# Performance work log

Measured on AMD Instinct MI355X. Metric: run time of the kernel, lower is better.

Reference implementation:

```python
import jax, jax.numpy as jnp
import numpy as np

B, C, H, W = 4, 64, 224, 224
WS = 14
HEADS = 4
HD = C // HEADS  # 16
N = WS * WS      # 196
SCALE = HD ** -0.5


def conv2d(x, w, b, pad):
    y = jax.lax.conv_general_dilated(x, w, (1, 1), [(pad, pad), (pad, pad)],
                                     dimension_numbers=('NCHW', 'OIHW', 'NCHW'))
    return y + b[None, :, None, None]


def layernorm(x, g, b, eps=1e-5):
    m = jnp.mean(x, axis=-1, keepdims=True)
    v = jnp.mean((x - m) ** 2, axis=-1, keepdims=True)
    return (x - m) * jax.lax.rsqrt(v + eps) * g + b


def window_partition(x):
    # x: (B,H,W,C) -> (B*nW, WS, WS, C)
    b, h, w, c = x.shape
    x = x.reshape(b, h // WS, WS, w // WS, WS, c)
    return x.transpose(0, 1, 3, 2, 4, 5).reshape(-1, WS, WS, c)


def window_reverse(win, h, w):
    b = win.shape[0] // ((h // WS) * (w // WS))
    x = win.reshape(b, h // WS, w // WS, WS, WS, -1)
    return x.transpose(0, 1, 3, 2, 4, 5).reshape(b, h, w, -1)


def setup_inputs():
    key = jax.random.key(0)
    ks = iter(jax.random.split(key, 64))
    nrm = lambda shp, s=0.02: (jax.random.normal(next(ks), shp, jnp.float32) * s)
    d = {}
    d['x'] = jax.random.normal(next(ks), (B, C, H, W), jnp.float32)
    d['x_basic'] = jax.random.normal(next(ks), (B, C, H, W), jnp.float32)
    # Aware_offset convs
    d['c1_w'] = nrm((64, 64, 3, 3)); d['c1_b'] = jnp.zeros((64,), jnp.float32)
    d['c2_w'] = nrm((64, 64, 5, 5)); d['c2_b'] = jnp.zeros((64,), jnp.float32)
    d['c3_w'] = nrm((64, 64, 7, 7)); d['c3_b'] = jnp.zeros((64,), jnp.float32)
    d['c4_w'] = nrm((64, 192, 3, 3)); d['c4_b'] = jnp.zeros((64,), jnp.float32)
    d['c5_w'] = nrm((128, 128, 3, 3)); d['c5_b'] = jnp.zeros((128,), jnp.float32)
    d['c6_w'] = nrm((128, 128, 3, 3)); d['c6_b'] = jnp.zeros((128,), jnp.float32)
    d['c7_w'] = nrm((64, 128, 1, 1)); d['c7_b'] = jnp.zeros((64,), jnp.float32)
    d['c8_w'] = nrm((64, 128, 1, 1)); d['c8_b'] = jnp.zeros((64,), jnp.float32)
    # block params
    d['qkv1_w'] = nrm((64, 64, 3, 3)); d['qkv1_b'] = jnp.zeros((64,), jnp.float32)
    d['n1_g'] = jnp.ones((C,), jnp.float32); d['n1_b'] = jnp.zeros((C,), jnp.float32)
    d['qkv_w'] = nrm((3 * C, C)); d['qkv_b'] = jnp.zeros((3 * C,), jnp.float32)
    d['corr_w'] = nrm((N, HD)); d['corr_b'] = jnp.zeros((N,), jnp.float32)
    d['proj_w'] = nrm((C, C)); d['proj_b'] = jnp.zeros((C,), jnp.float32)
    d['n2_g'] = jnp.ones((C,), jnp.float32); d['n2_b'] = jnp.zeros((C,), jnp.float32)
    d['fc1_w'] = nrm((2 * C, C)); d['fc1_b'] = jnp.zeros((2 * C,), jnp.float32)
    d['fc2_w'] = nrm((C, 2 * C)); d['fc2_b'] = jnp.zeros((C,), jnp.float32)
    return d


def _forward(x, x_basic, c1_w, c1_b, c2_w, c2_b, c3_w, c3_b, c4_w, c4_b,
             c5_w, c5_b, c6_w, c6_b, c7_w, c7_b, c8_w, c8_b,
             qkv1_w, qkv1_b, n1_g, n1_b, qkv_w, qkv_b, corr_w, corr_b,
             proj_w, proj_b, n2_g, n2_b, fc1_w, fc1_b, fc2_w, fc2_b):
    relu = jax.nn.relu
    # ---- Aware_offset ----
    in1 = relu(conv2d(x, c1_w, c1_b, 1))
    in2 = relu(conv2d(x, c2_w, c2_b, 2))
    in3 = relu(conv2d(x, c3_w, c3_b, 3))
    xo = relu(conv2d(jnp.concatenate([in1, in2, in3], 1), c4_w, c4_b, 1))
    cat12 = jnp.concatenate([x, x_basic], 1)
    b1 = relu(conv2d(cat12, c5_w, c5_b, 1))
    b2 = jax.nn.sigmoid(relu(conv2d(b1, c6_w, c6_b, 1)))
    b1 = relu(conv2d(b1 * b2, c7_w, c7_b, 0))
    xb = xo * b1 + relu(conv2d(cat12, c8_w, c8_b, 0))  # (B,C,H,W)
    xb = xb.transpose(0, 2, 3, 1)                       # (B,H,W,C)
    # ---- pre-attn: norm1 + convQKV1 ----
    xt = x.reshape(B, C, H * W).transpose(0, 2, 1)      # (B,L,C)
    xt = layernorm(xt, n1_g, n1_b)
    xc = xt.reshape(B, H, W, C).transpose(0, 3, 1, 2)
    xc = conv2d(xc, qkv1_w, qkv1_b, 1).transpose(0, 2, 3, 1)  # (B,H,W,C)
    # ---- windows ----
    xw = window_partition(xc).reshape(-1, N, C)   # (B_,N,C)
    xbw = window_partition(xb).reshape(-1, N, C)
    B_ = xw.shape[0]
    # ---- window attention with correction bias ----
    qkv = (xw @ qkv_w.T + qkv_b).reshape(B_, N, 3, HEADS, HD).transpose(2, 0, 3, 1, 4)
    q, k, v = qkv[0] * SCALE, qkv[1], qkv[2]            # (B_,h,N,hd)
    xcorr = xbw.reshape(B_, N, HEADS, HD).transpose(0, 2, 1, 3)
    xcorr = xcorr @ corr_w.T + corr_b                   # (B_,h,N,196)
    attn = jax.nn.softmax(jnp.einsum('bhnd,bhmd->bhnm', q, k) + xcorr, axis=-1)
    out = jnp.einsum('bhnm,bhmd->bhnd', attn, v).transpose(0, 2, 1, 3).reshape(B_, N, C)
    out = out @ proj_w.T + proj_b
    # ---- reverse + MLP ----
    sx = window_reverse(out.reshape(-1, WS, WS, C), H, W)  # (B,H,W,C)
    xt = sx.reshape(B, H * W, C)
    h = layernorm(xt, n2_g, n2_b)
    h = jax.nn.gelu(h @ fc1_w.T + fc1_b, approximate=False) @ fc2_w.T + fc2_b
    xt = xt + h
    return xt.reshape(B, H, W, C).transpose(0, 3, 1, 2)


def reference(x, x_basic, c1_w, c1_b, c2_w, c2_b, c3_w, c3_b, c4_w, c4_b,
              c5_w, c5_b, c6_w, c6_b, c7_w, c7_b, c8_w, c8_b,
              qkv1_w, qkv1_b, n1_g, n1_b, qkv_w, qkv_b, corr_w, corr_b,
              proj_w, proj_b, n2_g, n2_b, fc1_w, fc1_b, fc2_w, fc2_b):
    return _forward(x, x_basic, c1_w, c1_b, c2_w, c2_b, c3_w, c3_b, c4_w, c4_b,
                    c5_w, c5_b, c6_w, c6_b, c7_w, c7_b, c8_w, c8_b,
                    qkv1_w, qkv1_b, n1_g, n1_b, qkv_w, qkv_b, corr_w, corr_b,
                    proj_w, proj_b, n2_g, n2_b, fc1_w, fc1_b, fc2_w, fc2_b)
```

## Files before the change

### kernel.cpp

```cpp
#include <hip/hip_runtime.h>
#include <hip/hip_bf16.h>
#include <math.h>


#define HW  50176
#define WID 224

typedef unsigned short ushortT;
typedef __attribute__((ext_vector_type(8))) short bf8_t;
typedef __attribute__((ext_vector_type(4))) short bf4_t;
typedef __attribute__((ext_vector_type(4))) float f4_t;

__device__ __forceinline__ ushortT f2bf(float v) {
    __hip_bfloat16 h = __float2bfloat16(v);
    ushortT u; __builtin_memcpy(&u, &h, 2); return u;
}
__device__ __forceinline__ float bf2f(ushortT h) {
    union { float f; unsigned int u; } c; c.u = ((unsigned int)h) << 16;
    return c.f;
}
__device__ __forceinline__ void cvt8(const float* xv, bf8_t& hh, bf8_t& ll) {
    #pragma unroll
    for (int i = 0; i < 8; ++i) {
        ushortT hi = f2bf(xv[i]);
        hh[i] = (short)hi;
        ll[i] = (short)f2bf(xv[i] - bf2f(hi));
    }
}

__global__ __launch_bounds__(256) void packw(
    const float* __restrict__ w, ushortT* __restrict__ dst,
    int K, int IC, int OC, int total)
{
    int e = blockIdx.x * 256 + threadIdx.x;
    if (e >= total) return;
    int KK = K * K;
    int kk = e % KK; int rem = e / KK;
    int ic = rem % IC; int oc = rem / IC;
    float v = w[e];
    ushortT hi = f2bf(v);
    ushortT lo = f2bf(v - bf2f(hi));
    int g = oc >> 6, oc64 = oc & 63;
    int ic32 = ic >> 5, icin = ic & 31, kb = icin >> 3, ii = icin & 7;
    int nch = KK * (IC / 32);
    int chunk = ic32 * KK + kk;
    size_t base = ((size_t)(g * nch + chunk)) * 4096;
    dst[base + (kb * 64 + oc64) * 8 + ii] = hi;
    dst[base + 2048 + (kb * 64 + oc64) * 8 + ii] = lo;
}

template<int K>
__device__ __forceinline__ void convpass(
    const ushortT* __restrict__ wq, const ushortT* __restrict__ sm,
    int wv, int lc, int kb, f4_t (&ac)[2][4])
{
    constexpr int off = 3 - K / 2;
    constexpr int INSH = 14 * 22 * 40;
    const int boff = (kb * 64 + lc) * 8;
    bf8_t bh[4], bl[4];
    #pragma unroll
    for (int n = 0; n < 4; ++n) {
        bh[n] = *(const bf8_t*)(wq + boff + n * 128);
        bl[n] = *(const bf8_t*)(wq + 2048 + boff + n * 128);
    }
    #pragma unroll 1
    for (int kk = 0; kk < K * K; ++kk) {
        bf8_t cbh[4], cbl[4];
        #pragma unroll
        for (int n = 0; n < 4; ++n) { cbh[n] = bh[n]; cbl[n] = bl[n]; }
        if (kk + 1 < K * K) {
            const ushortT* wn = wq + (size_t)(kk + 1) * 4096;
            #pragma unroll
            for (int n = 0; n < 4; ++n) {
                bh[n] = *(const bf8_t*)(wn + boff + n * 128);
                bl[n] = *(const bf8_t*)(wn + 2048 + boff + n * 128);
            }
        }
        const int ky = kk / K, kx = kk % K;
        #pragma unroll
        for (int m = 0; m < 2; ++m) {
            const int row = 2 * wv + m + ky + off;
            const int col = lc + kx + off;
            const ushortT* ab = sm + (row * 22 + col) * 40 + kb * 8;
            bf8_t Ah = *(const bf8_t*)ab;
            bf8_t Al = *(const bf8_t*)(ab + INSH);
            #pragma unroll
            for (int n = 0; n < 4; ++n) {
                ac[m][n] = __builtin_amdgcn_mfma_f32_16x16x32_bf16(Ah, cbh[n], ac[m][n], 0, 0, 0);
                ac[m][n] = __builtin_amdgcn_mfma_f32_16x16x32_bf16(Ah, cbl[n], ac[m][n], 0, 0, 0);
                ac[m][n] = __builtin_amdgcn_mfma_f32_16x16x32_bf16(Al, cbh[n], ac[m][n], 0, 0, 0);
            }
        }
    }
}

__global__ __launch_bounds__(256, 4) void mfconv3(
    const float* __restrict__ in,
    const ushortT* __restrict__ w1p, const ushortT* __restrict__ w2p,
    const ushortT* __restrict__ w3p,
    const float* __restrict__ b1, const float* __restrict__ b2,
    const float* __restrict__ b3,
    float* __restrict__ out, int inStride, int outStride)
{
    constexpr int TWd = 22, THd = 14, ICP = 40;
    constexpr int INSH = THd * TWd * ICP;
    constexpr int E = THd * TWd * 32;
    __shared__ __align__(16) ushortT smem_u[2 * INSH];
    float* pool = (float*)smem_u;

    const int t = threadIdx.x, lane = t & 63, wv = t >> 6;
    const int lc = lane & 15, kb = lane >> 4;
    const int img = blockIdx.z;
    const int x0 = blockIdx.x * 16, y0 = blockIdx.y * 8;
    const float* inb = in + (size_t)img * inStride;

    f4_t acc1[2][4], acc2[2][4], acc3[2][4];
    {
        #pragma unroll
        for (int n = 0; n < 4; ++n) {
            float z1 = b1[n * 16 + lc], z2 = b2[n * 16 + lc], z3 = b3[n * 16 + lc];
            #pragma unroll
            for (int m = 0; m < 2; ++m) {
                acc1[m][n] = (f4_t){z1, z1, z1, z1};
                acc2[m][n] = (f4_t){z2, z2, z2, z2};
                acc3[m][n] = (f4_t){z3, z3, z3, z3};
            }
        }
    }

    #pragma unroll 1
    for (int ic32 = 0; ic32 < 2; ++ic32) {
        __syncthreads();
        #pragma unroll 1
        for (int ib = 0; ib < E; ib += 1024) {
            float v[4];
            #pragma unroll
            for (int u = 0; u < 4; ++u) {
                int i = ib + u * 256 + t;
                v[u] = 0.f;
                if (i < E) {
                    int icn = i / (THd * TWd);
                    int px  = i % (THd * TWd);
                    int ty = px / TWd, tx = px % TWd;
                    int gy = y0 + ty - 3, gx = x0 + tx - 3;
                    if (gy >= 0 && gy < WID && gx >= 0 && gx < WID)
                        v[u] = inb[(size_t)(ic32 * 32 + icn) * HW + gy * WID + gx];
                }
            }
            #pragma unroll
            for (int u = 0; u < 4; ++u) {
                int i = ib + u * 256 + t;
                if (i < E) {
                    int icn = i / (THd * TWd);
                    int px  = i % (THd * TWd);
                    ushortT hi = f2bf(v[u]);
                    smem_u[px * ICP + icn] = hi;
                    smem_u[INSH + px * ICP + icn] = f2bf(v[u] - bf2f(hi));
                }
            }
        }
        __syncthreads();
        convpass<3>(w1p + (size_t)(ic32 *  9) * 4096, smem_u, wv, lc, kb, acc1);
        convpass<5>(w2p + (size_t)(ic32 * 25) * 4096, smem_u, wv, lc, kb, acc2);
        convpass<7>(w3p + (size_t)(ic32 * 49) * 4096, smem_u, wv, lc, kb, acc3);
    }

    #pragma unroll 1
    for (int c = 0; c < 3; ++c) {
        float* ob0 = out + (size_t)img * outStride + (size_t)(c * 64) * HW;
        #pragma unroll
        for (int m = 0; m < 2; ++m) {
            __syncthreads();
            #pragma unroll
            for (int n = 0; n < 4; ++n)
                #pragma unroll
                for (int j = 0; j < 4; ++j) {
                    float v = (c == 0) ? acc1[m][n][j] : (c == 1) ? acc2[m][n][j] : acc3[m][n][j];
                    v = fmaxf(v, 0.f);
                    pool[(wv * 64 + n * 16 + lc) * 20 + kb * 4 + j] = v;
                }
            __syncthreads();
            {
                int rho = t >> 6, oc = t & 63;
                int y = y0 + 2 * rho + m;
                float* ob = ob0 + (size_t)oc * HW + (size_t)y * WID + x0;
                const float* pr = &pool[(rho * 64 + oc) * 20];
                #pragma unroll
                for (int c4 = 0; c4 < 4; ++c4) {
                    float4 st = { pr[c4*4+0], pr[c4*4+1], pr[c4*4+2], pr[c4*4+3] };
                    *(float4*)&ob[c4 * 4] = st;
                }
            }
        }
    }
}

template<int K, int IC, int OC, int ACT, bool CAT, bool LNRM, bool NHWCOUT>
__global__ __launch_bounds__(256, 4) void mfconv(
    const float* __restrict__ in, const float* __restrict__ in2,
    const ushortT* __restrict__ wpk, const float* __restrict__ bias,
    const float* __restrict__ mu, const float* __restrict__ rs,
    const float* __restrict__ lng, const float* __restrict__ lnb,
    float* __restrict__ out, int inStride, int outStride)
{
    constexpr int P = K / 2, TWd = 16 + K - 1, THd = 8 + K - 1, ICP = 40;
    constexpr int OCG = OC / 64, KK = K * K, NCH = KK * (IC / 32);
    constexpr int INSH = THd * TWd * ICP;
    constexpr int E = THd * TWd * 32;
    constexpr int SMU = (2 * INSH > 10240) ? 2 * INSH : 10240;
    __shared__ __align__(16) ushortT smem_u[SMU];
    float* pool = (float*)smem_u;

    const int t = threadIdx.x, lane = t & 63, wv = t >> 6;
    const int lc = lane & 15, kb = lane >> 4;
    const int img = blockIdx.z / OCG, g = blockIdx.z % OCG;
    const int x0 = blockIdx.x * 16, y0 = blockIdx.y * 8;
    const float* inb  = in + (size_t)img * inStride;
    const float* in2b = CAT ? (in2 + (size_t)img * inStride) : nullptr;
    const int imgPixBase = img * HW;
    const ushortT* wq0 = wpk + (size_t)g * NCH * 4096;

    f4_t acc[2][4];
    {
        float bz0 = bias[g * 64 +  0 + lc];
        float bz1 = bias[g * 64 + 16 + lc];
        float bz2 = bias[g * 64 + 32 + lc];
        float bz3 = bias[g * 64 + 48 + lc];
        #pragma unroll
        for (int m = 0; m < 2; ++m) {
            acc[m][0] = (f4_t){bz0, bz0, bz0, bz0};
            acc[m][1] = (f4_t){bz1, bz1, bz1, bz1};
            acc[m][2] = (f4_t){bz2, bz2, bz2, bz2};
            acc[m][3] = (f4_t){bz3, bz3, bz3, bz3};
        }
    }
    const int aoff = lc * ICP + kb * 8;
    const int boff = (kb * 64 + lc) * 8;

    #pragma unroll 1
    for (int ic32 = 0; ic32 < IC / 32; ++ic32) {
        __syncthreads();
        #pragma unroll 1
        for (int ib = 0; ib < E; ib += 1024) {
            float v[4];
            #pragma unroll
            for (int u = 0; u < 4; ++u) {
                int i = ib + u * 256 + t;
                v[u] = 0.f;
                if (i < E) {
                    int icn = i / (THd * TWd);
                    int px  = i % (THd * TWd);
                    int ty = px / TWd, tx = px % TWd;
                    int gy = y0 + ty - P, gx = x0 + tx - P;
                    int ic = ic32 * 32 + icn;
                    if (gy >= 0 && gy < WID && gx >= 0 && gx < WID) {
                        const float* s;
                        if (CAT) s = (ic < 64) ? (inb + (size_t)ic * HW)
                                               : (in2b + (size_t)(ic - 64) * HW);
                        else     s = inb + (size_t)ic * HW;
                        float vv = s[gy * WID + gx];
                        if (LNRM) {
                            int p = imgPixBase + gy * WID + gx;
                            vv = (vv - mu[p]) * rs[p] * lng[ic] + lnb[ic];
                        }
                        v[u] = vv;
                    }
                }
            }
            #pragma unroll
            for (int u = 0; u < 4; ++u) {
                int i = ib + u * 256 + t;
                if (i < E) {
                    int icn = i / (THd * TWd);
                    int px  = i % (THd * TWd);
                    ushortT hi = f2bf(v[u]);
                    smem_u[px * ICP + icn] = hi;
                    smem_u[INSH + px * ICP + icn] = f2bf(v[u] - bf2f(hi));
                }
            }
        }
        __syncthreads();
        const ushortT* wqb = wq0 + (size_t)(ic32 * KK) * 4096;
        bf8_t bh[4], bl[4];
        #pragma unroll
        for (int n = 0; n < 4; ++n) {
            bh[n] = *(const bf8_t*)(wqb + boff + n * 128);
            bl[n] = *(const bf8_t*)(wqb + 2048 + boff + n * 128);
        }
        #pragma unroll 1
        for (int kk = 0; kk < KK; ++kk) {
            bf8_t cbh[4], cbl[4];
            #pragma unroll
            for (int n = 0; n < 4; ++n) { cbh[n] = bh[n]; cbl[n] = bl[n]; }
            if (kk + 1 < KK) {
                const ushortT* wn = wqb + (size_t)(kk + 1) * 4096;
                #pragma unroll
                for (int n = 0; n < 4; ++n) {
                    bh[n] = *(const bf8_t*)(wn + boff + n * 128);
                    bl[n] = *(const bf8_t*)(wn + 2048 + boff + n * 128);
                }
            }
            const int ky = kk / K, kx = kk % K;
            #pragma unroll
            for (int m = 0; m < 2; ++m) {
                const int row = 2 * wv + m + ky;
                const ushortT* ab = smem_u + (row * TWd + kx) * ICP + aoff;
                bf8_t Ah = *(const bf8_t*)ab;
                bf8_t Al = *(const bf8_t*)(ab + INSH);
                #pragma unroll
                for (int n = 0; n < 4; ++n) {
                    acc[m][n] = __builtin_amdgcn_mfma_f32_16x16x32_bf16(Ah, cbh[n], acc[m][n], 0, 0, 0);
                    acc[m][n] = __builtin_amdgcn_mfma_f32_16x16x32_bf16(Ah, cbl[n], acc[m][n], 0, 0, 0);
                    acc[m][n] = __builtin_amdgcn_mfma_f32_16x16x32_bf16(Al, cbh[n], acc[m][n], 0, 0, 0);
                }
            }
        }
    }
    if (NHWCOUT) {
        float* ob0 = out + (size_t)img * outStride;
        #pragma unroll
        for (int m = 0; m < 2; ++m) {
            __syncthreads();
            #pragma unroll
            for (int n = 0; n < 4; ++n)
                #pragma unroll
                for (int j = 0; j < 4; ++j) {
                    float v = acc[m][n][j];
                    if (ACT == 1) v = fmaxf(v, 0.f);
                    else if (ACT == 2) v = 1.f / (1.f + __expf(-fmaxf(v, 0.f)));
                    pool[(wv * 16 + kb * 4 + j) * 68 + n * 16 + lc] = v;
                }
            __syncthreads();
            {
                int pix = t >> 2, q = t & 3;
                int y = y0 + 2 * (pix >> 4) + m;
                int x = x0 + (pix & 15);
                float* pr = ob0 + ((size_t)y * WID + x) * 64 + q * 16;
                const float* src = &pool[pix * 68 + q * 16];
                #pragma unroll
                for (int u = 0; u < 4; ++u)
                    *(float4*)&pr[u * 4] = *(const float4*)&src[u * 4];
            }
        }
    } else {
        float* ob0 = out + (size_t)img * outStride + (size_t)(g * 64) * HW;
        #pragma unroll
        for (int m = 0; m < 2; ++m) {
            __syncthreads();
            #pragma unroll
            for (int n = 0; n < 4; ++n)
                #pragma unroll
                for (int j = 0; j < 4; ++j) {
                    float v = acc[m][n][j];
                    if (ACT == 1) v = fmaxf(v, 0.f);
                    else if (ACT == 2) v = 1.f / (1.f + __expf(-fmaxf(v, 0.f)));
                    pool[(wv * 64 + n * 16 + lc) * 20 + kb * 4 + j] = v;
                }
            __syncthreads();
            {
                int rho = t >> 6, oc = t & 63;
                int y = y0 + 2 * rho + m;
                float* ob = ob0 + (size_t)oc * HW + (size_t)y * WID + x0;
                const float* pr = &pool[(rho * 64 + oc) * 20];
                #pragma unroll
                for (int c4 = 0; c4 < 4; ++c4) {
                    float4 st = { pr[c4*4+0], pr[c4*4+1], pr[c4*4+2], pr[c4*4+3] };
                    *(float4*)&ob[c4 * 4] = st;
                }
            }
        }
    }
}

__global__ __launch_bounds__(256) void ln_stats(
    const float* __restrict__ x, float* __restrict__ mu, float* __restrict__ rs)
{
    const int p = blockIdx.x * 256 + threadIdx.x;
    const int img = p / HW, pp = p - img * HW;
    const float* b = x + (size_t)img * 64 * HW + pp;
    float row[64];
    #pragma unroll
    for (int c = 0; c < 64; ++c) row[c] = b[(size_t)c * HW];
    float s1 = 0.f;
    #pragma unroll
    for (int c = 0; c < 64; ++c) s1 += row[c];
    float m = s1 * (1.f / 64.f);
    float s2 = 0.f;
    #pragma unroll
    for (int c = 0; c < 64; ++c) { float d = row[c] - m; s2 += d * d; }
    mu[p] = m;
    rs[p] = rsqrtf(s2 * (1.f / 64.f) + 1e-5f);
}

__global__ __launch_bounds__(256) void xb1x1(
    const float* __restrict__ x, const float* __restrict__ xbas,
    const float* __restrict__ xo, const float* __restrict__ b1, const float* __restrict__ b2,
    const float* __restrict__ c7w, const float* __restrict__ c7b,
    const float* __restrict__ c8w, const float* __restrict__ c8b,
    float* __restrict__ xbout)
{
    __shared__ __align__(16) float w7s[128 * 36], w8s[128 * 36];
    const int t = threadIdx.x, oh = blockIdx.y;
    for (int i = t; i < 4096; i += 256) {
        int o = i >> 7, ic = i & 127;
        w7s[ic * 36 + o] = c7w[(size_t)(oh * 32 + o) * 128 + ic];
        w8s[ic * 36 + o] = c8w[(size_t)(oh * 32 + o) * 128 + ic];
    }
    __syncthreads();
    const int p = blockIdx.x * 256 + t;
    const int img = p / HW, pp = p - img * HW;
    const float* b1p = b1 + (size_t)img * 128 * HW + pp;
    const float* b2p = b2 + (size_t)img * 128 * HW + pp;
    const float* xp  = x  + (size_t)img * 64 * HW + pp;
    const float* xbp = xbas + (size_t)img * 64 * HW + pp;
    float a7[32], a8[32];
    {
        const float4* c74 = (const float4*)(c7b + oh * 32);
        const float4* c84 = (const float4*)(c8b + oh * 32);
        #pragma unroll
        for (int j4 = 0; j4 < 8; ++j4) {
            float4 v7 = c74[j4], v8 = c84[j4];
            a7[j4*4+0]=v7.x; a7[j4*4+1]=v7.y; a7[j4*4+2]=v7.z; a7[j4*4+3]=v7.w;
            a8[j4*4+0]=v8.x; a8[j4*4+1]=v8.y; a8[j4*4+2]=v8.z; a8[j4*4+3]=v8.w;
        }
    }
    #pragma unroll 4
    for (int ic = 0; ic < 128; ++ic) {
        float tv = b1p[(size_t)ic * HW] * b2p[(size_t)ic * HW];
        float cv = (ic < 64) ? xp[(size_t)ic * HW] : xbp[(size_t)(ic - 64) * HW];
        const float4* w7r = (const float4*)&w7s[ic * 36];
        const float4* w8r = (const float4*)&w8s[ic * 36];
        #pragma unroll
        for (int j4 = 0; j4 < 8; ++j4) {
            float4 v7 = w7r[j4], v8 = w8r[j4];
            a7[j4*4+0] = fmaf(tv, v7.x, a7[j4*4+0]);
            a7[j4*4+1] = fmaf(tv, v7.y, a7[j4*4+1]);
            a7[j4*4+2] = fmaf(tv, v7.z, a7[j4*4+2]);
            a7[j4*4+3] = fmaf(tv, v7.w, a7[j4*4+3]);
            a8[j4*4+0] = fmaf(cv, v8.x, a8[j4*4+0]);
            a8[j4*4+1] = fmaf(cv, v8.y, a8[j4*4+1]);
            a8[j4*4+2] = fmaf(cv, v8.z, a8[j4*4+2]);
            a8[j4*4+3] = fmaf(cv, v8.w, a8[j4*4+3]);
        }
    }
    const float* xop = xo + (size_t)img * 64 * HW + pp;
    float* orow = xbout + (size_t)p * 64 + oh * 32;
    #pragma unroll
    for (int j4 = 0; j4 < 8; ++j4) {
        float4 st;
        st.x = xop[(size_t)(oh*32 + j4*4+0) * HW] * fmaxf(a7[j4*4+0], 0.f) + fmaxf(a8[j4*4+0], 0.f);
        st.y = xop[(size_t)(oh*32 + j4*4+1) * HW] * fmaxf(a7[j4*4+1], 0.f) + fmaxf(a8[j4*4+1], 0.f);
        st.z = xop[(size_t)(oh*32 + j4*4+2) * HW] * fmaxf(a7[j4*4+2], 0.f) + fmaxf(a8[j4*4+2], 0.f);
        st.w = xop[(size_t)(oh*32 + j4*4+3) * HW] * fmaxf(a7[j4*4+3], 0.f) + fmaxf(a8[j4*4+3], 0.f);
        *(float4*)&orow[j4 * 4] = st;
    }
}

__global__ __launch_bounds__(256) void attn(
    const float* __restrict__ xc, const float* __restrict__ xb,
    const float* __restrict__ qkvw, const float* __restrict__ qkvb,
    const float* __restrict__ corw, const float* __restrict__ corb,
    float* __restrict__ aout)
{
    constexpr int QS = 40;
    constexpr int VS = 212;
    __shared__ __align__(16) ushortT Kth[196 * QS];
    __shared__ __align__(16) ushortT Ktl[196 * QS];
    __shared__ __align__(16) ushortT Vth[16 * VS];
    __shared__ __align__(16) ushortT Vtl[16 * VS];
    __shared__ __align__(16) float CB[208];

    const int t = threadIdx.x;
    const int wdw = blockIdx.x >> 2, h = blockIdx.x & 3;
    const int b = wdw >> 8, wl = wdw & 255;
    const int wy = (wl >> 4) * 14, wx = (wl & 15) * 14;
    const int lane = t & 63, wv = t >> 6;
    const int g = lane >> 4, col = lane & 15;

    bf8_t Wqh[2], Wql[2], Wkh[2], Wkl[2], Wvh[2], Wvl[2];
    float qb[4], kb[4], vb[4];
    {
        #pragma unroll
        for (int ks = 0; ks < 2; ++ks) {
            float xv[8];
            const float* wr = qkvw + (h * 16 + col) * 64 + ks * 32 + g * 8;
            *(float4*)&xv[0] = *(const float4*)wr;
            *(float4*)&xv[4] = *(const float4*)(wr + 4);
            cvt8(xv, Wqh[ks], Wql[ks]);
            wr = qkvw + (64 + h * 16 + col) * 64 + ks * 32 + g * 8;
            *(float4*)&xv[0] = *(const float4*)wr;
            *(float4*)&xv[4] = *(const float4*)(wr + 4);
            cvt8(xv, Wkh[ks], Wkl[ks]);
            wr = qkvw + (128 + h * 16 + col) * 64 + ks * 32 + g * 8;
            *(float4*)&xv[0] = *(const float4*)wr;
            *(float4*)&xv[4] = *(const float4*)(wr + 4);
            cvt8(xv, Wvh[ks], Wvl[ks]);
        }
        float4 q4 = *(const float4*)(qkvb + h * 16 + g * 4);
        float4 k4 = *(const float4*)(qkvb + 64 + h * 16 + g * 4);
        float4 v4 = *(const float4*)(qkvb + 128 + h * 16 + g * 4);
        qb[0]=q4.x; qb[1]=q4.y; qb[2]=q4.z; qb[3]=q4.w;
        kb[0]=k4.x; kb[1]=k4.y; kb[2]=k4.z; kb[3]=k4.w;
        vb[0]=v4.x; vb[1]=v4.y; vb[2]=v4.z; vb[3]=v4.w;
    }

    if (t < 208) CB[t] = (t < 196) ? corb[t] : 0.f;
    if (t < 196) {
        unsigned* khr = (unsigned*)&Kth[t * QS];
        unsigned* klr = (unsigned*)&Ktl[t * QS];
        float xw[16];
        const float4* cw4 = (const float4*)(corw + t * 16);
        #pragma unroll
        for (int j = 0; j < 4; ++j) *(float4*)&xw[j * 4] = cw4[j];
        #pragma unroll
        for (int i = 0; i < 8; ++i) {
            ushortT ah = f2bf(xw[2*i]), bh = f2bf(xw[2*i+1]);
            ushortT al = f2bf(xw[2*i] - bf2f(ah)), bl = f2bf(xw[2*i+1] - bf2f(bh));
            khr[8 + i] = (unsigned)ah | ((unsigned)bh << 16);
            klr[8 + i] = (unsigned)al | ((unsigned)bl << 16);
        }
    }

    auto phaseB = [&](int mt) -> f4_t {
        const int row = 16 * mt + col;
        const int pix = (row > 195) ? 195 : row;
        const int rr = pix / 14, cc = pix - (pix / 14) * 14;
        const float* xr = xc + (size_t)((b * 224 + wy + rr) * 224 + wx + cc) * 64;
        f4_t dq = (f4_t){0.f, 0.f, 0.f, 0.f};
        f4_t dk = (f4_t){0.f, 0.f, 0.f, 0.f};
        f4_t dv = (f4_t){0.f, 0.f, 0.f, 0.f};
        #pragma unroll
        for (int ks = 0; ks < 2; ++ks) {
            float xv[8];
            *(float4*)&xv[0] = *(const float4*)(xr + ks * 32 + g * 8);
            *(float4*)&xv[4] = *(const float4*)(xr + ks * 32 + g * 8 + 4);
            bf8_t Xh, Xl;
            cvt8(xv, Xh, Xl);
            dq = __builtin_amdgcn_mfma_f32_16x16x32_bf16(Wqh[ks], Xh, dq, 0, 0, 0);
            dq = __builtin_amdgcn_mfma_f32_16x16x32_bf16(Wqh[ks], Xl, dq, 0, 0, 0);
            dq = __builtin_amdgcn_mfma_f32_16x16x32_bf16(Wql[ks], Xh, dq, 0, 0, 0);
            dk = __builtin_amdgcn_mfma_f32_16x16x32_bf16(Wkh[ks], Xh, dk, 0, 0, 0);
            dk = __builtin_amdgcn_mfma_f32_16x16x32_bf16(Wkh[ks], Xl, dk, 0, 0, 0);
            dk = __builtin_amdgcn_mfma_f32_16x16x32_bf16(Wkl[ks], Xh, dk, 0, 0, 0);
            dv = __builtin_amdgcn_mfma_f32_16x16x32_bf16(Wvh[ks], Xh, dv, 0, 0, 0);
            dv = __builtin_amdgcn_mfma_f32_16x16x32_bf16(Wvh[ks], Xl, dv, 0, 0, 0);
            dv = __builtin_amdgcn_mfma_f32_16x16x32_bf16(Wvl[ks], Xh, dv, 0, 0, 0);
        }
        #pragma unroll
        for (int j = 0; j < 4; ++j) {
            float v = dv[j] + vb[j];
            ushortT hi = f2bf(v);
            Vth[(g * 4 + j) * VS + row] = hi;
            Vtl[(g * 4 + j) * VS + row] = f2bf(v - bf2f(hi));
        }
        if (row < 196) {
            unsigned h0, h1, l0, l1;
            {
                float a = dk[0] + kb[0], bb = dk[1] + kb[1];
                ushortT ah = f2bf(a), bh = f2bf(bb);
                h0 = (unsigned)ah | ((unsigned)bh << 16);
                l0 = (unsigned)f2bf(a - bf2f(ah)) | ((unsigned)f2bf(bb - bf2f(bh)) << 16);
            }
            {
                float a = dk[2] + kb[2], bb = dk[3] + kb[3];
                ushortT ah = f2bf(a), bh = f2bf(bb);
                h1 = (unsigned)ah | ((unsigned)bh << 16);
                l1 = (unsigned)f2bf(a - bf2f(ah)) | ((unsigned)f2bf(bb - bf2f(bh)) << 16);
            }
            uint2 u;
            u.x = h0; u.y = h1; *(uint2*)&Kth[row * QS + g * 4] = u;
            u.x = l0; u.y = l1; *(uint2*)&Ktl[row * QS + g * 4] = u;
        }
        return (f4_t){(dq[0] + qb[0]) * 0.25f, (dq[1] + qb[1]) * 0.25f,
                      (dq[2] + qb[2]) * 0.25f, (dq[3] + qb[3]) * 0.25f};
    };

    f4_t dqs0 = phaseB(wv);
    f4_t dqs1 = phaseB(wv + 4);
    f4_t dqs2 = phaseB(wv + 8);
    f4_t dqs3 = (f4_t){0.f, 0.f, 0.f, 0.f};
    if (wv == 0) dqs3 = phaseB(12);
    __syncthreads();

    auto phaseC = [&](f4_t dqv, int qt) {
        const int row = 16 * qt + col;
        const int pixq = (row > 195) ? 195 : row;
        float q8[8];
        const int sl0 = ((2 * g) & 3) * 16 + col;
        const int sl1 = ((2 * g + 1) & 3) * 16 + col;
        q8[0] = __shfl(dqv[0], sl0); q8[1] = __shfl(dqv[1], sl0);
        q8[2] = __shfl(dqv[2], sl0); q8[3] = __shfl(dqv[3], sl0);
        q8[4] = __shfl(dqv[0], sl1); q8[5] = __shfl(dqv[1], sl1);
        q8[6] = __shfl(dqv[2], sl1); q8[7] = __shfl(dqv[3], sl1);
        if (g >= 2) {
            const int rr = pixq / 14, cc = pixq - (pixq / 14) * 14;
            const float* xr = xb + (size_t)((b * 224 + wy + rr) * 224 + wx + cc) * 64
                            + h * 16 + (g & 1) * 8;
            *(float4*)&q8[0] = *(const float4*)xr;
            *(float4*)&q8[4] = *(const float4*)(xr + 4);
        }
        bf8_t Bhf, Blf;
        cvt8(q8, Bhf, Blf);
        f4_t s[13];
        __builtin_amdgcn_s_setprio(1);
        #pragma unroll
        for (int kt = 0; kt < 13; ++kt) {
            const int krow = (16 * kt + col > 195) ? 195 : (16 * kt + col);
            const bf8_t Ahf = *(const bf8_t*)&Kth[krow * QS + g * 8];
            const bf8_t Alf = *(const bf8_t*)&Ktl[krow * QS + g * 8];
            f4_t a = (f4_t){0.f, 0.f, 0.f, 0.f};
            a = __builtin_amdgcn_mfma_f32_16x16x32_bf16(Ahf, Bhf, a, 0, 0, 0);
            a = __builtin_amdgcn_mfma_f32_16x16x32_bf16(Ahf, Blf, a, 0, 0, 0);
            a = __builtin_amdgcn_mfma_f32_16x16x32_bf16(Alf, Bhf, a, 0, 0, 0);
            const f4_t cb4 = *(const f4_t*)&CB[16 * kt + g * 4];
            s[kt] = a + cb4;
        }
        __builtin_amdgcn_s_setprio(0);
        if (g > 0) { s[12][0] = -3e38f; s[12][1] = -3e38f; s[12][2] = -3e38f; s[12][3] = -3e38f; }
        float mrow = -3e38f;
        #pragma unroll
        for (int kt = 0; kt < 13; ++kt)
            #pragma unroll
            for (int j = 0; j < 4; ++j) mrow = fmaxf(mrow, s[kt][j]);
        mrow = fmaxf(mrow, __shfl_xor(mrow, 16));
        mrow = fmaxf(mrow, __shfl_xor(mrow, 32));
        float lsum = 0.f;
        bf4_t ph[13], pl[13];
        #pragma unroll
        for (int kt = 0; kt < 13; ++kt) {
            #pragma unroll
            for (int j = 0; j < 4; ++j) {
                float p = __expf(s[kt][j] - mrow);
                lsum += p;
                ushortT hi = f2bf(p);
                ph[kt][j] = (short)hi;
                pl[kt][j] = (short)f2bf(p - bf2f(hi));
            }
        }
        lsum += __shfl_xor(lsum, 16);
        lsum += __shfl_xor(lsum, 32);
        f4_t o = (f4_t){0.f, 0.f, 0.f, 0.f};
        __builtin_amdgcn_s_setprio(1);
        #pragma unroll
        for (int kt = 0; kt < 13; ++kt) {
            const bf4_t vh = *(const bf4_t*)&Vth[col * VS + 16 * kt + g * 4];
            const bf4_t vl = *(const bf4_t*)&Vtl[col * VS + 16 * kt + g * 4];
            o = __builtin_amdgcn_mfma_f32_16x16x16bf16_1k(vh, ph[kt], o, 0, 0, 0);
            o = __builtin_amdgcn_mfma_f32_16x16x16bf16_1k(vl, ph[kt], o, 0, 0, 0);
            o = __builtin_amdgcn_mfma_f32_16x16x16bf16_1k(vh, pl[kt], o, 0, 0, 0);
        }
        __builtin_amdgcn_s_setprio(0);
        const int pix = 16 * qt + col;
        if (pix < 196) {
            const float inv = 1.f / lsum;
            const int rr = pix / 14, cc = pix % 14;
            const size_t pixIdx = (size_t)((b * 224 + wy + rr) * 224 + wx + cc);
            float4 st = { o[0] * inv, o[1] * inv, o[2] * inv, o[3] * inv };
            *(float4*)&aout[pixIdx * 64 + h * 16 + g * 4] = st;
        }
    };

    phaseC(dqs0, wv);
    phaseC(dqs1, wv + 4);
    phaseC(dqs2, wv + 8);
    if (wv == 0) phaseC(dqs3, 12);
}

__global__ __launch_bounds__(256) void mlpproj(
    const float* __restrict__ aout,
    const float* __restrict__ pw, const float* __restrict__ pbias,
    const float* __restrict__ g, const float* __restrict__ be,
    const float* __restrict__ fc1w, const float* __restrict__ fc1b,
    const float* __restrict__ fc2w, const float* __restrict__ fc2b,
    float* __restrict__ out)
{
    __shared__ __align__(16) float pwT[64 * 68];
    __shared__ __align__(16) float w1[4096], w2t[4096];
    const int t = threadIdx.x;
    for (int i = t; i < 4096; i += 256) {
        int o = i >> 6, c = i & 63;
        pwT[c * 68 + o] = pw[i];
    }
    __syncthreads();
    const int p = blockIdx.x * 256 + t;
    const float* ar = aout + (size_t)p * 64;
    float srow[64];
    {
        const float4* pb4 = (const float4*)pbias;
        #pragma unroll
        for (int j4 = 0; j4 < 16; ++j4) {
            float4 v = pb4[j4];
            srow[j4*4+0]=v.x; srow[j4*4+1]=v.y; srow[j4*4+2]=v.z; srow[j4*4+3]=v.w;
        }
    }
    const float4* ar4 = (const float4*)ar;
    #pragma unroll 2
    for (int c4 = 0; c4 < 16; ++c4) {
        float4 av = ar4[c4];
        const float4* w0 = (const float4*)&pwT[(c4 * 4 + 0) * 68];
        const float4* wB = (const float4*)&pwT[(c4 * 4 + 1) * 68];
        const float4* wC = (const float4*)&pwT[(c4 * 4 + 2) * 68];
        const float4* wD = (const float4*)&pwT[(c4 * 4 + 3) * 68];
        #pragma unroll
        for (int j4 = 0; j4 < 16; ++j4) {
            float4 a0 = w0[j4], a1 = wB[j4], a2 = wC[j4], a3 = wD[j4];
            srow[j4*4+0] = fmaf(av.x, a0.x, fmaf(av.y, a1.x, fmaf(av.z, a2.x, fmaf(av.w, a3.x, srow[j4*4+0]))));
            srow[j4*4+1] = fmaf(av.x, a0.y, fmaf(av.y, a1.y, fmaf(av.z, a2.y, fmaf(av.w, a3.y, srow[j4*4+1]))));
            srow[j4*4+2] = fmaf(av.x, a0.z, fmaf(av.y, a1.z, fmaf(av.z, a2.z, fmaf(av.w, a3.z, srow[j4*4+2]))));
            srow[j4*4+3] = fmaf(av.x, a0.w, fmaf(av.y, a1.w, fmaf(av.z, a2.w, fmaf(av.w, a3.w, srow[j4*4+3]))));
        }
    }
    float s1 = 0.f;
    #pragma unroll
    for (int c = 0; c < 64; ++c) s1 += srow[c];
    float m = s1 * (1.f / 64.f);
    float s2 = 0.f;
    #pragma unroll
    for (int c = 0; c < 64; ++c) { float d = srow[c] - m; s2 += d * d; }
    float rstd = rsqrtf(s2 * (1.f / 64.f) + 1e-5f);
    float nrow[64];
    {
        const float4* g4 = (const float4*)g;
        const float4* b4 = (const float4*)be;
        #pragma unroll
        for (int j4 = 0; j4 < 16; ++j4) {
            float4 gv = g4[j4], bv = b4[j4];
            nrow[j4*4+0] = (srow[j4*4+0] - m) * rstd * gv.x + bv.x;
            nrow[j4*4+1] = (srow[j4*4+1] - m) * rstd * gv.y + bv.y;
            nrow[j4*4+2] = (srow[j4*4+2] - m) * rstd * gv.z + bv.z;
            nrow[j4*4+3] = (srow[j4*4+3] - m) * rstd * gv.w + bv.w;
        }
    }
    float acc[64];
    {
        const float4* f2b4 = (const float4*)fc2b;
        #pragma unroll
        for (int j4 = 0; j4 < 16; ++j4) {
            float4 v = f2b4[j4];
            acc[j4*4+0]=v.x; acc[j4*4+1]=v.y; acc[j4*4+2]=v.z; acc[j4*4+3]=v.w;
        }
    }
    for (int half = 0; half < 2; ++half) {
        __syncthreads();
        for (int i = t; i < 4096; i += 256) {
            int j = i >> 6, c = i & 63;
            w1[i]  = fc1w[(half * 64 + j) * 64 + c];
            w2t[i] = fc2w[c * 128 + half * 64 + j];
        }
        __syncthreads();
        #pragma unroll 1
        for (int j = 0; j < 64; ++j) {
            const float4* wr = (const float4*)&w1[j * 64];
            float d0 = 0, d1 = 0, d2 = 0, d3 = 0;
            #pragma unroll
            for (int c4 = 0; c4 < 16; ++c4) {
                float4 wv = wr[c4];
                d0 = fmaf(nrow[c4*4+0], wv.x, d0); d1 = fmaf(nrow[c4*4+1], wv.y, d1);
                d2 = fmaf(nrow[c4*4+2], wv.z, d2); d3 = fmaf(nrow[c4*4+3], wv.w, d3);
            }
            float hv = fc1b[half * 64 + j] + ((d0 + d1) + (d2 + d3));
            float gl = 0.5f * hv * (1.f + erff(hv * 0.70710678118f));
            const float4* w2r = (const float4*)&w2t[j * 64];
            #pragma unroll
            for (int c4 = 0; c4 < 16; ++c4) {
                float4 wv = w2r[c4];
                acc[c4*4+0] = fmaf(gl, wv.x, acc[c4*4+0]);
                acc[c4*4+1] = fmaf(gl, wv.y, acc[c4*4+1]);
                acc[c4*4+2] = fmaf(gl, wv.z, acc[c4*4+2]);
                acc[c4*4+3] = fmaf(gl, wv.w, acc[c4*4+3]);
            }
        }
    }
    const int img = p / HW, pp = p - img * HW;
    float* ob = out + (size_t)img * 64 * HW + pp;
    #pragma unroll
    for (int c = 0; c < 64; ++c)
        ob[(size_t)c * HW] = srow[c] + acc[c];
}

extern "C" void kernel_launch(void* const* d_in, const int* in_sizes, int n_in,
                              void* d_out, int out_size, void* d_ws, size_t ws_size,
                              hipStream_t stream)
{
    (void)in_sizes; (void)n_in; (void)out_size;
    const float* x      = (const float*)d_in[0];
    const float* xbasic = (const float*)d_in[1];
    const float* c1w  = (const float*)d_in[2];  const float* c1b  = (const float*)d_in[3];
    const float* c2w  = (const float*)d_in[4];  const float* c2b  = (const float*)d_in[5];
    const float* c3w  = (const float*)d_in[6];  const float* c3b  = (const float*)d_in[7];
    const float* c4w  = (const float*)d_in[8];  const float* c4b  = (const float*)d_in[9];
    const float* c5w  = (const float*)d_in[10]; const float* c5b  = (const float*)d_in[11];
    const float* c6w  = (const float*)d_in[12]; const float* c6b  = (const float*)d_in[13];
    const float* c7w  = (const float*)d_in[14]; const float* c7b  = (const float*)d_in[15];
    const float* c8w  = (const float*)d_in[16]; const float* c8b  = (const float*)d_in[17];
    const float* qk1w = (const float*)d_in[18]; const float* qk1b = (const float*)d_in[19];
    const float* n1g  = (const float*)d_in[20]; const float* n1b  = (const float*)d_in[21];
    const float* qkvw = (const float*)d_in[22]; const float* qkvb = (const float*)d_in[23];
    const float* corw = (const float*)d_in[24]; const float* corb = (const float*)d_in[25];
    const float* prjw = (const float*)d_in[26]; const float* prjb = (const float*)d_in[27];
    const float* n2g  = (const float*)d_in[28]; const float* n2b  = (const float*)d_in[29];
    const float* f1w  = (const float*)d_in[30]; const float* f1b  = (const float*)d_in[31];
    const float* f2w  = (const float*)d_in[32]; const float* f2b  = (const float*)d_in[33];

    float* ws = (float*)d_ws;
    const size_t SCR0 = 26836992ull;
    const size_t need4 = (SCR0 + 4ull * 19267584ull) * 4ull;
    const size_t need2 = (SCR0 + 2ull * 19267584ull) * 4ull;
    const int CS = (ws_size >= need4) ? 4 : (ws_size >= need2) ? 2 : 1;
    const int nch = 4 / CS;

    float* XC = ws;
    float* XB = ws + 12845056;
    float* MU = ws + 25690112;
    float* RS = ws + 25890816;
    ushortT* WP = (ushortT*)(ws + 26091520);
    float* A  = ws + SCR0;
    float* XO = A + (size_t)CS * 9633792;
    float* B1 = XO + (size_t)CS * 3211264;
    float* B2 = A;
    float* AOUT = A;
    ushortT* WQ1 = (ushortT*)B1;

    const size_t o1 = 0, o2 = 73728, o3 = 278528, o4 = 679936, o5 = 901120, o6 = 1196032;

    ln_stats<<<784, 256, 0, stream>>>(x, MU, RS);

    {
        auto PK = [&](const float* w, ushortT* dst, int K, int IC, int OC) {
            int tot = OC * IC * K * K;
            packw<<<(tot + 255) / 256, 256, 0, stream>>>(w, dst, K, IC, OC, tot);
        };
        PK(qk1w, WQ1, 3, 64, 64);
        PK(c1w, WP + o1, 3, 64, 64);
        PK(c2w, WP + o2, 5, 64, 64);
        PK(c3w, WP + o3, 7, 64, 64);
        PK(c4w, WP + o4, 3, 192, 64);
        PK(c5w, WP + o5, 3, 128, 128);
        PK(c6w, WP + o6, 3, 128, 128);
    }

    mfconv<3, 64, 64, 0, false, true, true><<<dim3(14, 28, 4), 256, 0, stream>>>(
        x, nullptr, WQ1, qk1b, MU, RS, n1g, n1b, XC, 64 * HW, HW * 64);

    for (int ch = 0; ch < nch; ++ch) {
        const float* xi  = x      + (size_t)ch * CS * 64 * HW;
        const float* xbi = xbasic + (size_t)ch * CS * 64 * HW;
        mfconv3<<<dim3(14, 28, CS), 256, 0, stream>>>(
            xi, WP + o1, WP + o2, WP + o3, c1b, c2b, c3b, A, 64 * HW, 192 * HW);
        mfconv<3, 192, 64, 1, false, false, false><<<dim3(14, 28, CS), 256, 0, stream>>>(
            A, nullptr, WP + o4, c4b, nullptr, nullptr, nullptr, nullptr, XO, 192 * HW, 64 * HW);
        mfconv<3, 128, 128, 1, true, false, false><<<dim3(14, 28, CS * 2), 256, 0, stream>>>(
            xi, xbi, WP + o5, c5b, nullptr, nullptr, nullptr, nullptr, B1, 64 * HW, 128 * HW);
        mfconv<3, 128, 128, 2, false, false, false><<<dim3(14, 28, CS * 2), 256, 0, stream>>>(
            B1, nullptr, WP + o6, c6b, nullptr, nullptr, nullptr, nullptr, B2, 128 * HW, 128 * HW);
        xb1x1<<<dim3(CS * 196, 2), 256, 0, stream>>>(
            xi, xbi, XO, B1, B2, c7w, c7b, c8w, c8b, XB + (size_t)ch * CS * HW * 64);
    }

    attn<<<4096, 256, 0, stream>>>(XC, XB, qkvw, qkvb, corw, corb, AOUT);
    mlpproj<<<784, 256, 0, stream>>>(AOUT, prjw, prjb, n2g, n2b, f1w, f1b, f2w, f2b,
                                     (float*)d_out);
}
```

Measured before the change: 1.917 ms.

## Rewrite proj+LN+MLP tail on MFMA with split-bf16 prepacked weights

Replaces the scalar-FMA per-pixel projection, LayerNorm and GELU MLP kernel with an MFMA version. Each wave handles 16 pixels and uses split-bf16 (hi/lo, three products) to keep near-fp32 accuracy. The LayerNorm reduction moves to cross-lane shuffles, and the weights are prepacked into MFMA fragment layout by new small pack kernels, stored in the freed MU buffer. The aim is to cut the large VALU cost of the three 64/128-wide matmuls. In exchange it adds extra MFMA work for the split precision, plus strided output stores.

After: 1.778 ms (median of 2 runs). 1.08x faster.

```diff
diff --git a/kernel.cpp b/kernel.cpp
--- a/kernel.cpp
+++ b/kernel.cpp
@@ -47,6 +47,36 @@
     size_t base = ((size_t)(g * nch + chunk)) * 4096;
     dst[base + (kb * 64 + oc64) * 8 + ii] = hi;
     dst[base + 2048 + (kb * 64 + oc64) * 8 + ii] = lo;
+}
+
+__global__ __launch_bounds__(256) void packa32(
+    const float* __restrict__ w, ushortT* __restrict__ dst, int K, int total)
+{
+    int e = blockIdx.x * 256 + threadIdx.x;
+    if (e >= total) return;
+    int f = e >> 9, r = e & 511, ln = r >> 3, i = r & 7;
+    int nk = K >> 5;
+    int o = f / nk, ks = f % nk;
+    int c = ln & 15, gg = ln >> 4;
+    float v = w[(size_t)(o * 16 + c) * K + ks * 32 + gg * 8 + i];
+    ushortT hi = f2bf(v);
+    dst[(size_t)f * 1024 + ln * 8 + i] = hi;
+    dst[(size_t)f * 1024 + 512 + ln * 8 + i] = f2bf(v - bf2f(hi));
+}
+
+__global__ __launch_bounds__(256) void packa16(
+    const float* __restrict__ w, ushortT* __restrict__ dst, int K, int total)
+{
+    int e = blockIdx.x * 256 + threadIdx.x;
+    if (e >= total) return;
+    int f = e >> 8, r = e & 255, ln = r >> 2, i = r & 3;
+    int nk = K >> 4;
+    int o = f / nk, n = f % nk;
+    int c = ln & 15, gg = ln >> 4;
+    float v = w[(size_t)(o * 16 + c) * K + n * 16 + gg * 4 + i];
+    ushortT hi = f2bf(v);
+    dst[(size_t)f * 512 + ln * 4 + i] = hi;
+    dst[(size_t)f * 512 + 256 + ln * 4 + i] = f2bf(v - bf2f(hi));
 }
 
 template<int K>
@@ -666,116 +696,120 @@
     if (wv == 0) phaseC(dqs3, 12);
 }
 
-__global__ __launch_bounds__(256) void mlpproj(
-    const float* __restrict__ aout,
-    const float* __restrict__ pw, const float* __restrict__ pbias,
-    const float* __restrict__ g, const float* __restrict__ be,
-    const float* __restrict__ fc1w, const float* __restrict__ fc1b,
-    const float* __restrict__ fc2w, const float* __restrict__ fc2b,
+__global__ __launch_bounds__(256) void mlpmf(
+    const float* __restrict__ aout, const ushortT* __restrict__ pk,
+    const float* __restrict__ pbias,
+    const float* __restrict__ lng, const float* __restrict__ lnb,
+    const float* __restrict__ fc1b, const float* __restrict__ fc2b,
     float* __restrict__ out)
 {
-    __shared__ __align__(16) float pwT[64 * 68];
-    __shared__ __align__(16) float w1[4096], w2t[4096];
-    const int t = threadIdx.x;
-    for (int i = t; i < 4096; i += 256) {
-        int o = i >> 6, c = i & 63;
-        pwT[c * 68 + o] = pw[i];
-    }
-    __syncthreads();
-    const int p = blockIdx.x * 256 + t;
-    const float* ar = aout + (size_t)p * 64;
-    float srow[64];
-    {
-        const float4* pb4 = (const float4*)pbias;
-        #pragma unroll
-        for (int j4 = 0; j4 < 16; ++j4) {
-            float4 v = pb4[j4];
-            srow[j4*4+0]=v.x; srow[j4*4+1]=v.y; srow[j4*4+2]=v.z; srow[j4*4+3]=v.w;
-        }
-    }
-    const float4* ar4 = (const float4*)ar;
-    #pragma unroll 2
-    for (int c4 = 0; c4 < 16; ++c4) {
-        float4 av = ar4[c4];
-        const float4* w0 = (const float4*)&pwT[(c4 * 4 + 0) * 68];
-        const float4* wB = (const float4*)&pwT[(c4 * 4 + 1) * 68];
-        const float4* wC = (const float4*)&pwT[(c4 * 4 + 2) * 68];
-        const float4* wD = (const float4*)&pwT[(c4 * 4 + 3) * 68];
-        #pragma unroll
-        for (int j4 = 0; j4 < 16; ++j4) {
-            float4 a0 = w0[j4], a1 = wB[j4], a2 = wC[j4], a3 = wD[j4];
-            srow[j4*4+0] = fmaf(av.x, a0.x, fmaf(av.y, a1.x, fmaf(av.z, a2.x, fmaf(av.w, a3.x, srow[j4*4+0]))));
-            srow[j4*4+1] = fmaf(av.x, a0.y, fmaf(av.y, a1.y, fmaf(av.z, a2.y, fmaf(av.w, a3.y, srow[j4*4+1]))));
-            srow[j4*4+2] = fmaf(av.x, a0.z, fmaf(av.y, a1.z, fmaf(av.z, a2.z, fmaf(av.w, a3.z, srow[j4*4+2]))));
-            srow[j4*4+3] = fmaf(av.x, a0.w, fmaf(av.y, a1.w, fmaf(av.z, a2.w, fmaf(av.w, a3.w, srow[j4*4+3]))));
-        }
-    }
-    float s1 = 0.f;
-    #pragma unroll
-    for (int c = 0; c < 64; ++c) s1 += srow[c];
-    float m = s1 * (1.f / 64.f);
-    float s2 = 0.f;
-    #pragma unroll
-    for (int c = 0; c < 64; ++c) { float d = srow[c] - m; s2 += d * d; }
-    float rstd = rsqrtf(s2 * (1.f / 64.f) + 1e-5f);
-    float nrow[64];
-    {
-        const float4* g4 = (const float4*)g;
-        const float4* b4 = (const float4*)be;
-        #pragma unroll
-        for (int j4 = 0; j4 < 16; ++j4) {
-            float4 gv = g4[j4], bv = b4[j4];
-            nrow[j4*4+0] = (srow[j4*4+0] - m) * rstd * gv.x + bv.x;
-            nrow[j4*4+1] = (srow[j4*4+1] - m) * rstd * gv.y + bv.y;
-            nrow[j4*4+2] = (srow[j4*4+2] - m) * rstd * gv.z + bv.z;
-            nrow[j4*4+3] = (srow[j4*4+3] - m) * rstd * gv.w + bv.w;
-        }
-    }
-    float acc[64];
-    {
-        const float4* f2b4 = (const float4*)fc2b;
-        #pragma unroll
-        for (int j4 = 0; j4 < 16; ++j4) {
-            float4 v = f2b4[j4];
-            acc[j4*4+0]=v.x; acc[j4*4+1]=v.y; acc[j4*4+2]=v.z; acc[j4*4+3]=v.w;
-        }
-    }
-    for (int half = 0; half < 2; ++half) {
-        __syncthreads();
-        for (int i = t; i < 4096; i += 256) {
-            int j = i >> 6, c = i & 63;
-            w1[i]  = fc1w[(half * 64 + j) * 64 + c];
-            w2t[i] = fc2w[c * 128 + half * 64 + j];
-        }
-        __syncthreads();
-        #pragma unroll 1
-        for (int j = 0; j < 64; ++j) {
-            const float4* wr = (const float4*)&w1[j * 64];
-            float d0 = 0, d1 = 0, d2 = 0, d3 = 0;
-            #pragma unroll
-            for (int c4 = 0; c4 < 16; ++c4) {
-                float4 wv = wr[c4];
-                d0 = fmaf(nrow[c4*4+0], wv.x, d0); d1 = fmaf(nrow[c4*4+1], wv.y, d1);
-                d2 = fmaf(nrow[c4*4+2], wv.z, d2); d3 = fmaf(nrow[c4*4+3], wv.w, d3);
-            }
-            float hv = fc1b[half * 64 + j] + ((d0 + d1) + (d2 + d3));
+    const int t = threadIdx.x, lane = t & 63, wv = t >> 6;
+    const int gq = lane >> 4, col = lane & 15;
+    const int p0 = (blockIdx.x * 4 + wv) * 16;
+    const ushortT* pk1 = pk;
+    const ushortT* pk2 = pk + 8192;
+    const ushortT* pk3 = pk + 24576;
+
+    f4_t S[4];
+    #pragma unroll
+    for (int n = 0; n < 4; ++n) {
+        float4 b4 = *(const float4*)(pbias + n * 16 + gq * 4);
+        S[n] = (f4_t){b4.x, b4.y, b4.z, b4.w};
+    }
+    const float* xr = aout + (size_t)(p0 + col) * 64;
+    #pragma unroll
+    for (int ks = 0; ks < 2; ++ks) {
+        float xv[8];
+        *(float4*)&xv[0] = *(const float4*)(xr + ks * 32 + gq * 8);
+        *(float4*)&xv[4] = *(const float4*)(xr + ks * 32 + gq * 8 + 4);
+        bf8_t Xh, Xl;
+        cvt8(xv, Xh, Xl);
+        #pragma unroll
+        for (int n = 0; n < 4; ++n) {
+            const ushortT* a = pk1 + (size_t)(n * 2 + ks) * 1024 + lane * 8;
+            bf8_t Ah = *(const bf8_t*)a;
+            bf8_t Al = *(const bf8_t*)(a + 512);
+            S[n] = __builtin_amdgcn_mfma_f32_16x16x32_bf16(Ah, Xh, S[n], 0, 0, 0);
+            S[n] = __builtin_amdgcn_mfma_f32_16x16x32_bf16(Ah, Xl, S[n], 0, 0, 0);
+            S[n] = __builtin_amdgcn_mfma_f32_16x16x32_bf16(Al, Xh, S[n], 0, 0, 0);
+        }
+    }
+    float sum = 0.f;
+    #pragma unroll
+    for (int n = 0; n < 4; ++n)
+        #pragma unroll
+        for (int j = 0; j < 4; ++j) sum += S[n][j];
+    sum += __shfl_xor(sum, 16);
+    sum += __shfl_xor(sum, 32);
+    float mean = sum * (1.f / 64.f);
+    float var = 0.f;
+    #pragma unroll
+    for (int n = 0; n < 4; ++n)
+        #pragma unroll
+        for (int j = 0; j < 4; ++j) { float d = S[n][j] - mean; var += d * d; }
+    var += __shfl_xor(var, 16);
+    var += __shfl_xor(var, 32);
+    float rstd = rsqrtf(var * (1.f / 64.f) + 1e-5f);
+    bf4_t Nh[4], Nl[4];
+    #pragma unroll
+    for (int n = 0; n < 4; ++n) {
+        float4 g4 = *(const float4*)(lng + n * 16 + gq * 4);
+        float4 b4 = *(const float4*)(lnb + n * 16 + gq * 4);
+        float nv0 = (S[n][0] - mean) * rstd * g4.x + b4.x;
+        float nv1 = (S[n][1] - mean) * rstd * g4.y + b4.y;
+        float nv2 = (S[n][2] - mean) * rstd * g4.z + b4.z;
+        float nv3 = (S[n][3] - mean) * rstd * g4.w + b4.w;
+        ushortT h0 = f2bf(nv0), h1 = f2bf(nv1), h2 = f2bf(nv2), h3 = f2bf(nv3);
+        Nh[n][0] = (short)h0; Nh[n][1] = (short)h1; Nh[n][2] = (short)h2; Nh[n][3] = (short)h3;
+        Nl[n][0] = (short)f2bf(nv0 - bf2f(h0));
+        Nl[n][1] = (short)f2bf(nv1 - bf2f(h1));
+        Nl[n][2] = (short)f2bf(nv2 - bf2f(h2));
+        Nl[n][3] = (short)f2bf(nv3 - bf2f(h3));
+    }
+    bf4_t Gh[8], Gl[8];
+    #pragma unroll
+    for (int o = 0; o < 8; ++o) {
+        float4 b4 = *(const float4*)(fc1b + o * 16 + gq * 4);
+        f4_t hacc = (f4_t){b4.x, b4.y, b4.z, b4.w};
+        #pragma unroll
+        for (int n = 0; n < 4; ++n) {
+            const ushortT* a = pk2 + (size_t)(o * 4 + n) * 512 + lane * 4;
+            bf4_t Ah = *(const bf4_t*)a;
+            bf4_t Al = *(const bf4_t*)(a + 256);
+            hacc = __builtin_amdgcn_mfma_f32_16x16x16bf16_1k(Ah, Nh[n], hacc, 0, 0, 0);
+            hacc = __builtin_amdgcn_mfma_f32_16x16x16bf16_1k(Ah, Nl[n], hacc, 0, 0, 0);
+            hacc = __builtin_amdgcn_mfma_f32_16x16x16bf16_1k(Al, Nh[n], hacc, 0, 0, 0);
+        }
+        #pragma unroll
+        for (int j = 0; j < 4; ++j) {
+            float hv = hacc[j];
             float gl = 0.5f * hv * (1.f + erff(hv * 0.70710678118f));
-            const float4* w2r = (const float4*)&w2t[j * 64];
-            #pragma unroll
-            for (int c4 = 0; c4 < 16; ++c4) {
-                float4 wv = w2r[c4];
-                acc[c4*4+0] = fmaf(gl, wv.x, acc[c4*4+0]);
-                acc[c4*4+1] = fmaf(gl, wv.y, acc[c4*4+1]);
-                acc[c4*4+2] = fmaf(gl, wv.z, acc[c4*4+2]);
-                acc[c4*4+3] = fmaf(gl, wv.w, acc[c4*4+3]);
-            }
-        }
-    }
-    const int img = p / HW, pp = p - img * HW;
-    float* ob = out + (size_t)img * 64 * HW + pp;
-    #pragma unroll
-    for (int c = 0; c < 64; ++c)
-        ob[(size_t)c * HW] = srow[c] + acc[c];
+            ushortT hi = f2bf(gl);
+            Gh[o][j] = (short)hi;
+            Gl[o][j] = (short)f2bf(gl - bf2f(hi));
+        }
+    }
+    const int img = p0 / HW, pp = p0 - img * HW;
+    float* ob = out + (size_t)img * 64 * HW + pp + col;
+    #pragma unroll
+    for (int o2 = 0; o2 < 4; ++o2) {
+        float4 b4 = *(const float4*)(fc2b + o2 * 16 + gq * 4);
+        f4_t oacc = (f4_t){b4.x, b4.y, b4.z, b4.w};
+        #pragma unroll
+        for (int k2 = 0; k2 < 8; ++k2) {
+            const ushortT* a = pk3 + (size_t)(o2 * 8 + k2) * 512 + lane * 4;
+            bf4_t Ah = *(const bf4_t*)a;
+            bf4_t Al = *(const bf4_t*)(a + 256);
+            oacc = __builtin_amdgcn_mfma_f32_16x16x16bf16_1k(Ah, Gh[k2], oacc, 0, 0, 0);
+            oacc = __builtin_amdgcn_mfma_f32_16x16x16bf16_1k(Ah, Gl[k2], oacc, 0, 0, 0);
+            oacc = __builtin_amdgcn_mfma_f32_16x16x16bf16_1k(Al, Gh[k2], oacc, 0, 0, 0);
+        }
+        #pragma unroll
+        for (int j = 0; j < 4; ++j) {
+            int och = o2 * 16 + gq * 4 + j;
+            ob[(size_t)och * HW] = S[o2][j] + oacc[j];
+        }
+    }
 }
 
 extern "C" void kernel_launch(void* const* d_in, const int* in_sizes, int n_in,
@@ -820,6 +854,7 @@
     float* B2 = A;
     float* AOUT = A;
     ushortT* WQ1 = (ushortT*)B1;
+    ushortT* PM  = (ushortT*)MU;
 
     const size_t o1 = 0, o2 = 73728, o3 = 278528, o4 = 679936, o5 = 901120, o6 = 1196032;
 
@@ -841,6 +876,10 @@
 
     mfconv<3, 64, 64, 0, false, true, true><<<dim3(14, 28, 4), 256, 0, stream>>>(
         x, nullptr, WQ1, qk1b, MU, RS, n1g, n1b, XC, 64 * HW, HW * 64);
+
+    packa32<<<16, 256, 0, stream>>>(prjw, PM, 64, 4096);
+    packa16<<<32, 256, 0, stream>>>(f1w, PM + 8192, 64, 8192);
+    packa16<<<32, 256, 0, stream>>>(f2w, PM + 24576, 128, 8192);
 
     for (int ch = 0; ch < nch; ++ch) {
         const float* xi  = x      + (size_t)ch * CS * 64 * HW;
@@ -858,6 +897,6 @@
     }
 
     attn<<<4096, 256, 0, stream>>>(XC, XB, qkvw, qkvb, corw, corb, AOUT);
-    mlpproj<<<784, 256, 0, stream>>>(AOUT, prjw, prjb, n2g, n2b, f1w, f1b, f2w, f2b,
-                                     (float*)d_out);
-}
+    mlpmf<<<3136, 256, 0, stream>>>(AOUT, PM, prjb, n2g, n2b, f1b, f2b,
+                                    (float*)d_out);
+}
```
